# Performance work log

Measured on AMD Instinct MI355X. Metric: run time of the kernel, lower is better.

## Reference

```python
import jax, jax.numpy as jnp
import numpy as np

E = 2048        # embed_dim
H = 16          # num_heads
HKV = 4         # num_heads_kv (GQA)
D = 128         # head_dim
DCONV = 4       # causal depthwise conv width
ROT_DIM = 128   # rotary_emb_dim (= head_dim, full rotation)
ROT_BASE = 10000.0
QKV_DIM = D * (H + 2 * HKV)  # 3072
B, S = 2, 2048


def setup_inputs() -> dict:
    key = jax.random.key(0)
    ks = jax.random.split(key, 7)
    return {
        "x": jax.random.normal(ks[0], (B, S, E), jnp.float32),
        "W_in": jax.random.normal(ks[1], (E, QKV_DIM), jnp.float32) * 0.02,
        "b_in": jax.random.normal(ks[2], (QKV_DIM,), jnp.float32) * 0.02,
        "conv_w": jax.random.normal(ks[3], (QKV_DIM, DCONV), jnp.float32) * 0.1,
        "conv_b": jax.random.normal(ks[4], (QKV_DIM,), jnp.float32) * 0.02,
        "W_out": jax.random.normal(ks[5], (E, E), jnp.float32) * 0.02,
        "b_out": jax.random.normal(ks[6], (E,), jnp.float32) * 0.02,
    }


def _rotary_cos_sin(seqlen, dtype):
    # flash_attn RotaryEmbedding: inv_freq over even indices
    inv_freq = 1.0 / (ROT_BASE ** (np.arange(0, ROT_DIM, 2, dtype=np.float32) / ROT_DIM))
    t = np.arange(seqlen, dtype=np.float32)
    freqs = np.outer(t, inv_freq)                      # [S, ROT_DIM/2]
    return jnp.asarray(np.cos(freqs), dtype), jnp.asarray(np.sin(freqs), dtype)


def _apply_rotary(xh, cos, sin):
    # non-interleaved: rotate halves of the first ROT_DIM dims. xh: [B,S,h,D]
    x1 = xh[..., : ROT_DIM // 2]
    x2 = xh[..., ROT_DIM // 2 : ROT_DIM]
    c = cos[None, :, None, :]
    s = sin[None, :, None, :]
    rot = jnp.concatenate([x1 * c - x2 * s, x2 * c + x1 * s], axis=-1)
    return jnp.concatenate([rot, xh[..., ROT_DIM:]], axis=-1)


def _forward(x, W_in, b_in, conv_w, conv_b, W_out, b_out):
    b, s, _ = x.shape
    qkv = x @ W_in + b_in                              # [B,S,QKV_DIM]

    # causal depthwise conv1d (kernel DCONV, left-pad DCONV-1, trim right)
    xp = jnp.pad(qkv, ((0, 0), (DCONV - 1, 0), (0, 0)))
    conv = conv_b
    for k in range(DCONV):
        conv = conv + xp[:, k : k + s, :] * conv_w[:, k]
    qkv = conv                                         # [B,S,QKV_DIM]

    q, kv = jnp.split(qkv, [H * D], axis=-1)
    q = q.reshape(b, s, H, D)
    kv = kv.reshape(b, s, 2, HKV, D)
    k, v = kv[:, :, 0], kv[:, :, 1]                    # [B,S,HKV,D]

    cos, sin = _rotary_cos_sin(s, x.dtype)
    q = _apply_rotary(q, cos, sin)
    k = _apply_rotary(k, cos, sin)

    # GQA: repeat kv heads
    rep = H // HKV
    k = jnp.repeat(k, rep, axis=2)                     # [B,S,H,D]
    v = jnp.repeat(v, rep, axis=2)

    scale = 1.0 / np.sqrt(D)
    scores = jnp.einsum("bqhd,bkhd->bhqk", q, k) * scale
    causal = jnp.tril(jnp.ones((s, s), bool))
    scores = jnp.where(causal[None, None], scores, jnp.finfo(scores.dtype).min)
    probs = jax.nn.softmax(scores, axis=-1)
    ctx = jnp.einsum("bhqk,bkhd->bqhd", probs, v)      # [B,S,H,D]

    return ctx.reshape(b, s, H * D) @ W_out + b_out    # [B,S,E]


def reference(x, W_in, b_in, conv_w, conv_b, W_out, b_out):
    return _forward(x, W_in, b_in, conv_w, conv_b, W_out, b_out)
```

## Files before the change

### kernel.cpp

```cpp
#include <hip/hip_runtime.h>
#include <hip/hip_bf16.h>

#define B_    2
#define S_    2048
#define E_    2048
#define H_    16
#define HKV_  4
#define D_    128
#define QKV_  3072

#define LOG2E  1.4426950408889634f
#define SCALE  0.08838834764831845f
#define SL     0.127517431f

typedef __attribute__((ext_vector_type(8))) short short8;
typedef __attribute__((ext_vector_type(4))) float floatx4;

typedef __attribute__((address_space(1))) const unsigned int gu32;
typedef __attribute__((address_space(3))) unsigned int lu32;

__device__ __forceinline__ void load_lds16(const unsigned short* g, unsigned short* l) {
    __builtin_amdgcn_global_load_lds((gu32*)g, (lu32*)l, 16, 0, 0);
}

__device__ __forceinline__ float b2f(unsigned short u) {
    union { unsigned int i; float f; } v; v.i = ((unsigned int)u) << 16; return v.f;
}
__device__ __forceinline__ unsigned short f2b(float f) {
    union { float f; unsigned int i; } v; v.f = f;
    unsigned int r = v.i + 0x7FFFu + ((v.i >> 16) & 1u);
    return (unsigned short)(r >> 16);
}
__device__ __forceinline__ unsigned int fbits(float f) {
    union { float f; unsigned int i; } v; v.f = f; return v.i;
}
__device__ __forceinline__ float bits2f(unsigned int i) {
    union { unsigned int i; float f; } v; v.i = i; return v.f;
}

__global__ __launch_bounds__(256) void cvt_f32_bf16(
    const float* __restrict__ src, unsigned short* __restrict__ dst, int n)
{
    int i = (blockIdx.x * 256 + threadIdx.x) * 4;
    if (i + 3 < n) {
        float4 v = *(const float4*)&src[i];
        ushort4 o;
        o.x = f2b(v.x); o.y = f2b(v.y); o.z = f2b(v.z); o.w = f2b(v.w);
        *(ushort4*)&dst[i] = o;
    }
}

__global__ __launch_bounds__(256) void transpose_f32_bf16(
    const float* __restrict__ src, unsigned short* __restrict__ dst,
    int R, int C)
{
    __shared__ unsigned short tile[32][33];
    const int c0 = blockIdx.x * 32, r0 = blockIdx.y * 32;
    const int tx = threadIdx.x, ty = threadIdx.y;
    #pragma unroll
    for (int i = 0; i < 4; i++)
        tile[ty + 8 * i][tx] = f2b(src[(size_t)(r0 + ty + 8 * i) * C + c0 + tx]);
    __syncthreads();
    #pragma unroll
    for (int i = 0; i < 4; i++)
        dst[(size_t)(c0 + ty + 8 * i) * R + r0 + tx] = tile[tx][ty + 8 * i];
}

__global__ __launch_bounds__(256) void transpose_bf16(
    const unsigned short* __restrict__ src, unsigned short* __restrict__ dst,
    int R, int C)
{
    __shared__ unsigned short tile[32][33];
    const size_t boff = (size_t)blockIdx.z * R * C;
    src += boff; dst += boff;
    const int c0 = blockIdx.x * 32, r0 = blockIdx.y * 32;
    const int tx = threadIdx.x, ty = threadIdx.y;
    #pragma unroll
    for (int i = 0; i < 4; i++)
        tile[ty + 8 * i][tx] = src[(size_t)(r0 + ty + 8 * i) * C + c0 + tx];
    __syncthreads();
    #pragma unroll
    for (int i = 0; i < 4; i++)
        dst[(size_t)(c0 + ty + 8 * i) * R + r0 + tx] = tile[tx][ty + 8 * i];
}

template<int OUTF32>
__global__ __launch_bounds__(256) void gemm_bt(
    const unsigned short* __restrict__ A, const unsigned short* __restrict__ Bt,
    const float* __restrict__ bias, void* __restrict__ Cv,
    int M, int N, int K)
{
    __shared__ unsigned short As[128 * 64];
    __shared__ unsigned short Bs[128 * 64];
    const int tid = threadIdx.x;
    const int m0 = blockIdx.y * 128, n0 = blockIdx.x * 128;
    const int wave = tid >> 6, lane = tid & 63, ln = lane & 15, kq = lane >> 4;
    const int wm = (wave >> 1) * 64, wn = (wave & 1) * 64;

    floatx4 acc[4][4];
    #pragma unroll
    for (int i = 0; i < 4; i++)
        #pragma unroll
        for (int j = 0; j < 4; j++) {
            acc[i][j][0] = 0.f; acc[i][j][1] = 0.f; acc[i][j][2] = 0.f; acc[i][j][3] = 0.f;
        }

    const int lrow = lane >> 3;
    const int lcol = (lane & 7) * 8;

    for (int k0 = 0; k0 < K; k0 += 64) {
        __syncthreads();
        #pragma unroll
        for (int c = 0; c < 4; c++) {
            int rbase = wave * 32 + c * 8;
            int row = rbase + lrow;
            load_lds16(&A [(size_t)(m0 + row) * K + k0 + lcol], &As[rbase * 64]);
            load_lds16(&Bt[(size_t)(n0 + row) * K + k0 + lcol], &Bs[rbase * 64]);
        }
        __syncthreads();
        #pragma unroll
        for (int ks = 0; ks < 2; ks++) {
            short8 af[4], bg[4];
            #pragma unroll
            for (int i = 0; i < 4; i++)
                af[i] = *(const short8*)&As[(wm + i * 16 + ln) * 64 + ks * 32 + kq * 8];
            #pragma unroll
            for (int j = 0; j < 4; j++)
                bg[j] = *(const short8*)&Bs[(wn + j * 16 + ln) * 64 + ks * 32 + kq * 8];
            #pragma unroll
            for (int i = 0; i < 4; i++)
                #pragma unroll
                for (int j = 0; j < 4; j++)
                    acc[i][j] = __builtin_amdgcn_mfma_f32_16x16x32_bf16(af[i], bg[j], acc[i][j], 0, 0, 0);
        }
    }

    #pragma unroll
    for (int j = 0; j < 4; j++) {
        int col = n0 + wn + j * 16 + ln;
        float bv = bias[col];
        #pragma unroll
        for (int i = 0; i < 4; i++) {
            int rowb = m0 + wm + i * 16 + kq * 4;
            #pragma unroll
            for (int r = 0; r < 4; r++) {
                float val = acc[i][j][r] + bv;
                if (OUTF32) ((float*)Cv)[(size_t)(rowb + r) * N + col] = val;
                else ((unsigned short*)Cv)[(size_t)(rowb + r) * N + col] = f2b(val);
            }
        }
    }
}

__device__ __forceinline__ float conv_at(
    const unsigned short* __restrict__ qb, const float* __restrict__ cw,
    const float* __restrict__ cb, int s, int c)
{
    float acc = cb[c];
    const float* w = cw + c * 4;
    #pragma unroll
    for (int t = 0; t < 4; t++) {
        int sp = s - 3 + t;
        if (sp >= 0) acc += b2f(qb[(size_t)sp * QKV_ + c]) * w[t];
    }
    return acc;
}

__global__ __launch_bounds__(256) void conv_rot(
    const unsigned short* __restrict__ qkv, const float* __restrict__ cw,
    const float* __restrict__ cb, unsigned short* __restrict__ qo,
    unsigned short* __restrict__ ko, unsigned short* __restrict__ vo)
{
    const int bs = blockIdx.x;
    const int b = bs >> 11, s = bs & 2047;
    const unsigned short* qb = qkv + (size_t)b * S_ * QKV_;

    for (int it = threadIdx.x; it < 1792; it += 256) {
        if (it < 1280) {
            const int isq = it < 1024;
            const int rel = isq ? it : it - 1024;
            const int head = rel >> 6, d = rel & 63;
            const int c1 = (isq ? head * 128 : 2048 + head * 128) + d;
            float x1 = conv_at(qb, cw, cb, s, c1);
            float x2 = conv_at(qb, cw, cb, s, c1 + 64);
            float inv = exp2f((float)d * -0.2076205059304601f);
            float ang = (float)s * inv;
            float sn, cs;
            __sincosf(ang, &sn, &cs);
            float r1 = x1 * cs - x2 * sn;
            float r2 = x2 * cs + x1 * sn;
            unsigned short* dst = isq
                ? qo + ((size_t)(b * H_   + head) * S_ + s) * D_
                : ko + ((size_t)(b * HKV_ + head) * S_ + s) * D_;
            dst[d]      = f2b(r1);
            dst[d + 64] = f2b(r2);
        } else {
            const int idx = it - 1280;
            const int g = idx >> 7, d = idx & 127;
            float vv = conv_at(qb, cw, cb, s, 2560 + idx);
            vo[((size_t)(b * HKV_ + g) * S_ + s) * D_ + d] = f2b(vv);
        }
    }
}

__global__ __launch_bounds__(256, 4) void attn(
    const unsigned short* __restrict__ q, const unsigned short* __restrict__ k,
    const unsigned short* __restrict__ vT, unsigned short* __restrict__ ctx)
{
    __shared__ unsigned short Ks[64 * 128];
    __shared__ unsigned short Vs[128 * 64];
    __shared__ unsigned short Ps[4][16][64];

    const int h = blockIdx.x, qt = 31 - blockIdx.y, b = blockIdx.z, g = h >> 2;
    const int tid = threadIdx.x, wave = tid >> 6, lane = tid & 63;
    const int ln = lane & 15, kq = lane >> 4;

    const unsigned short* qh = q  + (size_t)(b * H_   + h) * S_ * D_;
    const unsigned short* kh = k  + (size_t)(b * HKV_ + g) * S_ * D_;
    const unsigned short* vh = vT + (size_t)(b * HKV_ + g) * D_ * S_;

    const int rK = (lane >> 4);
    const int pK = lane & 15;
    const int rV = (lane >> 3);
    const int pV = lane & 7;

    const int qrow0 = qt * 64 + wave * 16;

    short8 qf[4];
    #pragma unroll
    for (int f = 0; f < 4; f++)
        qf[f] = *(const short8*)&qh[(size_t)(qrow0 + ln) * D_ + f * 32 + kq * 8];

    floatx4 o[8];
    #pragma unroll
    for (int i = 0; i < 8; i++) { o[i][0] = 0.f; o[i][1] = 0.f; o[i][2] = 0.f; o[i][3] = 0.f; }
    float mr = -INFINITY, lr = 0.f;

    for (int kt = 0; kt <= qt; kt++) {
        __syncthreads();
        #pragma unroll
        for (int c = 0; c < 4; c++) {
            const int chunk = wave * 4 + c;
            int r  = chunk * 4 + rK;
            int gc = pK ^ (r & 15);
            load_lds16(&kh[(size_t)(kt * 64 + r) * D_ + gc * 8], &Ks[chunk * 512]);
            int rv = chunk * 8 + rV;
            int gv = pV ^ (rv & 7);
            load_lds16(&vh[(size_t)rv * S_ + kt * 64 + gv * 8], &Vs[chunk * 512]);
        }
        __syncthreads();

        floatx4 scv[4];
        #pragma unroll
        for (int nb = 0; nb < 4; nb++) { scv[nb][0]=0.f; scv[nb][1]=0.f; scv[nb][2]=0.f; scv[nb][3]=0.f; }
        #pragma unroll
        for (int ks = 0; ks < 4; ks++) {
            #pragma unroll
            for (int nb = 0; nb < 4; nb++) {
                short8 kf = *(const short8*)&Ks[(nb * 16 + ln) * 128 + (((ks * 4 + kq) ^ ln) * 8)];
                scv[nb] = __builtin_amdgcn_mfma_f32_16x16x32_bf16(kf, qf[ks], scv[nb], 0, 0, 0);
            }
        }

        if (kt == qt) {
            const int qloc = wave * 16 + ln;
            #pragma unroll
            for (int nb = 0; nb < 4; nb++)
                #pragma unroll
                for (int r = 0; r < 4; r++)
                    if (nb * 16 + kq * 4 + r > qloc) scv[nb][r] = -INFINITY;
        }

        float mx = -INFINITY;
        #pragma unroll
        for (int nb = 0; nb < 4; nb++) {
            float a0 = fmaxf(scv[nb][0], scv[nb][1]);
            float a1 = fmaxf(scv[nb][2], scv[nb][3]);
            mx = fmaxf(mx, fmaxf(a0, a1));
        }
        mx = fmaxf(mx, __shfl_xor(mx, 16));
        mx = fmaxf(mx, __shfl_xor(mx, 32));
        float mt = fmaxf(mr, mx);
        float al = exp2f((mr - mt) * SL);
        mr = mt;

        float rs = 0.f;
        #pragma unroll
        for (int nb = 0; nb < 4; nb++) {
            const int gct = 2 * nb + (kq >> 1);
            const int pbase = ((gct ^ (ln & 7)) << 3) + ((kq & 1) << 2);
            #pragma unroll
            for (int rr = 0; rr < 2; rr++) {
                unsigned int u0 = fbits(exp2f((scv[nb][2 * rr]     - mt) * SL));
                unsigned int u1 = fbits(exp2f((scv[nb][2 * rr + 1] - mt) * SL));
                rs += bits2f(u0 & 0xFFFF0000u) + bits2f(u1 & 0xFFFF0000u);
                *(unsigned int*)&Ps[wave][ln][pbase + 2 * rr] =
                    (u0 >> 16) | (u1 & 0xFFFF0000u);
            }
        }
        rs += __shfl_xor(rs, 16);
        rs += __shfl_xor(rs, 32);
        lr = lr * al + rs;

        float alr[4];
        #pragma unroll
        for (int r = 0; r < 4; r++) alr[r] = __shfl(al, kq * 4 + r);
        #pragma unroll
        for (int dn = 0; dn < 8; dn++)
            #pragma unroll
            for (int r = 0; r < 4; r++) o[dn][r] *= alr[r];

        short8 pa0 = *(const short8*)&Ps[wave][ln][(kq ^ (ln & 7)) << 3];
        short8 pa1 = *(const short8*)&Ps[wave][ln][((4 + kq) ^ (ln & 7)) << 3];
        #pragma unroll
        for (int dn = 0; dn < 8; dn++) {
            short8 b0 = *(const short8*)&Vs[(dn * 16 + ln) * 64 + ((kq ^ (ln & 7)) * 8)];
            o[dn] = __builtin_amdgcn_mfma_f32_16x16x32_bf16(pa0, b0, o[dn], 0, 0, 0);
            short8 b1 = *(const short8*)&Vs[(dn * 16 + ln) * 64 + (((4 + kq) ^ (ln & 7)) * 8)];
            o[dn] = __builtin_amdgcn_mfma_f32_16x16x32_bf16(pa1, b1, o[dn], 0, 0, 0);
        }
    }

    float lrr[4];
    #pragma unroll
    for (int r = 0; r < 4; r++) lrr[r] = 1.0f / __shfl(lr, kq * 4 + r);
    #pragma unroll
    for (int r = 0; r < 4; r++) {
        size_t rowoff = (size_t)(b * S_ + qt * 64 + wave * 16 + kq * 4 + r) * (H_ * D_) + h * D_;
        #pragma unroll
        for (int dn = 0; dn < 8; dn++)
            ctx[rowoff + dn * 16 + ln] = f2b(o[dn][r] * lrr[r]);
    }
}

extern "C" void kernel_launch(void* const* d_in, const int* in_sizes, int n_in,
                              void* d_out, int out_size, void* d_ws, size_t ws_size,
                              hipStream_t stream)
{
    const float* x     = (const float*)d_in[0];
    const float* W_in  = (const float*)d_in[1];
    const float* b_in  = (const float*)d_in[2];
    const float* cw    = (const float*)d_in[3];
    const float* cb    = (const float*)d_in[4];
    const float* W_out = (const float*)d_in[5];
    const float* b_out = (const float*)d_in[6];
    float* out = (float*)d_out;
    char* ws = (char*)d_ws;

    const size_t MB = 1024 * 1024;
    unsigned short* WtIn  = (unsigned short*)(ws);
    unsigned short* WtOut = (unsigned short*)(ws + 12 * MB);
    unsigned short* x16   = (unsigned short*)(ws + 20 * MB);
    unsigned short* qkv   = (unsigned short*)(ws + 36 * MB);
    unsigned short* qa    = (unsigned short*)(ws + 60 * MB);
    unsigned short* ka    = (unsigned short*)(ws + 76 * MB);
    unsigned short* va    = (unsigned short*)(ws + 80 * MB);
    unsigned short* vTa   = (unsigned short*)(ws + 84 * MB);
    unsigned short* ctx   = (unsigned short*)(ws + 20 * MB);

    dim3 tb(32, 8);
    hipLaunchKernelGGL(cvt_f32_bf16, dim3(8192), dim3(256), 0, stream, x, x16, 8388608);
    hipLaunchKernelGGL(transpose_f32_bf16, dim3(96, 64), tb, 0, stream, W_in,  WtIn,  2048, 3072);
    hipLaunchKernelGGL(transpose_f32_bf16, dim3(64, 64), tb, 0, stream, W_out, WtOut, 2048, 2048);
    hipLaunchKernelGGL(gemm_bt<0>, dim3(24, 32), dim3(256), 0, stream, x16, WtIn, b_in, (void*)qkv, 4096, 3072, 2048);
    hipLaunchKernelGGL(conv_rot, dim3(4096), dim3(256), 0, stream, qkv, cw, cb, qa, ka, va);
    hipLaunchKernelGGL(transpose_bf16, dim3(4, 64, 8), tb, 0, stream, va, vTa, 2048, 128);
    hipLaunchKernelGGL(attn, dim3(16, 32, 2), dim3(256), 0, stream, qa, ka, vTa, ctx);
    hipLaunchKernelGGL(gemm_bt<1>, dim3(16, 32), dim3(256), 0, stream, ctx, WtOut, b_out, (void*)out, 4096, 2048, 2048);
}
```

Baseline: 411.0 us.

## Replace GEMM with 8-wave double-buffered pipelined kernel with swizzled LDS

Replaces the simple 128x128 single-buffered GEMM with an 8-wave, 256-row tile kernel that double-buffers LDS. Global-to-LDS loads for the next K-tile are staged in four sub-units interleaved with MFMA work on quadrants of the current tile, using explicit vmcnt waits and barriers. It also XOR-swizzles LDS columns to avoid bank conflicts, remaps workgroup IDs for cache locality and raises MFMA priority. The aim is to hide memory latency and raise MFMA utilisation in both projection GEMMs. The cost is larger tiles, more LDS and register pressure, and fewer workgroups.

```diff
diff --git a/kernel.cpp b/kernel.cpp
--- a/kernel.cpp
+++ b/kernel.cpp
@@ -38,6 +38,19 @@
     union { unsigned int i; float f; } v; v.i = i; return v.f;
 }
 
+template<int N> __device__ __forceinline__ void waitcnt_vm() {
+    static_assert(N >= 0 && N <= 8, "vmcnt out of range");
+    if constexpr (N == 0) asm volatile("s_waitcnt vmcnt(0)" ::: "memory");
+    else if constexpr (N == 1) asm volatile("s_waitcnt vmcnt(1)" ::: "memory");
+    else if constexpr (N == 2) asm volatile("s_waitcnt vmcnt(2)" ::: "memory");
+    else if constexpr (N == 3) asm volatile("s_waitcnt vmcnt(3)" ::: "memory");
+    else if constexpr (N == 4) asm volatile("s_waitcnt vmcnt(4)" ::: "memory");
+    else if constexpr (N == 5) asm volatile("s_waitcnt vmcnt(5)" ::: "memory");
+    else if constexpr (N == 6) asm volatile("s_waitcnt vmcnt(6)" ::: "memory");
+    else if constexpr (N == 7) asm volatile("s_waitcnt vmcnt(7)" ::: "memory");
+    else asm volatile("s_waitcnt vmcnt(8)" ::: "memory");
+}
+
 __global__ __launch_bounds__(256) void cvt_f32_bf16(
     const float* __restrict__ src, unsigned short* __restrict__ dst, int n)
 {
@@ -84,67 +97,153 @@
         dst[(size_t)(c0 + ty + 8 * i) * R + r0 + tx] = tile[tx][ty + 8 * i];
 }
 
-template<int OUTF32>
-__global__ __launch_bounds__(256) void gemm_bt(
+template<int WR, int QR, int LX>
+__device__ __forceinline__ void stage_unit8(
+    const unsigned short* __restrict__ G, unsigned short* ls,
+    int uu, int g0, int K, int k0, int wave, int lane)
+{
+    #pragma unroll
+    for (int l = 0; l < LX; ++l) {
+        const int c    = wave * LX + l;
+        const int rr   = c / (QR / 8);
+        const int row0 = rr * WR + uu * QR + (c % (QR / 8)) * 8;
+        const int srow = row0 + (lane >> 3);
+        const int sg   = (lane & 7) ^ (lane >> 3);
+        load_lds16(&G[(size_t)(g0 + srow) * K + k0 + sg * 8], &ls[row0 * 64]);
+    }
+}
+
+template<int BN, int WM, int WN, int OUTF32>
+__global__ __launch_bounds__(512, 2) void gemm8(
     const unsigned short* __restrict__ A, const unsigned short* __restrict__ Bt,
     const float* __restrict__ bias, void* __restrict__ Cv,
     int M, int N, int K)
 {
-    __shared__ unsigned short As[128 * 64];
-    __shared__ unsigned short Bs[128 * 64];
-    const int tid = threadIdx.x;
-    const int m0 = blockIdx.y * 128, n0 = blockIdx.x * 128;
-    const int wave = tid >> 6, lane = tid & 63, ln = lane & 15, kq = lane >> 4;
-    const int wm = (wave >> 1) * 64, wn = (wave & 1) * 64;
-
-    floatx4 acc[4][4];
-    #pragma unroll
-    for (int i = 0; i < 4; i++)
-        #pragma unroll
-        for (int j = 0; j < 4; j++) {
-            acc[i][j][0] = 0.f; acc[i][j][1] = 0.f; acc[i][j][2] = 0.f; acc[i][j][3] = 0.f;
-        }
-
-    const int lrow = lane >> 3;
-    const int lcol = (lane & 7) * 8;
-
-    for (int k0 = 0; k0 < K; k0 += 64) {
-        __syncthreads();
-        #pragma unroll
-        for (int c = 0; c < 4; c++) {
-            int rbase = wave * 32 + c * 8;
-            int row = rbase + lrow;
-            load_lds16(&A [(size_t)(m0 + row) * K + k0 + lcol], &As[rbase * 64]);
-            load_lds16(&Bt[(size_t)(n0 + row) * K + k0 + lcol], &Bs[rbase * 64]);
-        }
-        __syncthreads();
-        #pragma unroll
-        for (int ks = 0; ks < 2; ks++) {
-            short8 af[4], bg[4];
-            #pragma unroll
-            for (int i = 0; i < 4; i++)
-                af[i] = *(const short8*)&As[(wm + i * 16 + ln) * 64 + ks * 32 + kq * 8];
-            #pragma unroll
-            for (int j = 0; j < 4; j++)
-                bg[j] = *(const short8*)&Bs[(wn + j * 16 + ln) * 64 + ks * 32 + kq * 8];
-            #pragma unroll
-            for (int i = 0; i < 4; i++)
-                #pragma unroll
-                for (int j = 0; j < 4; j++)
-                    acc[i][j] = __builtin_amdgcn_mfma_f32_16x16x32_bf16(af[i], bg[j], acc[i][j], 0, 0, 0);
-        }
-    }
-
-    #pragma unroll
-    for (int j = 0; j < 4; j++) {
-        int col = n0 + wn + j * 16 + ln;
-        float bv = bias[col];
-        #pragma unroll
-        for (int i = 0; i < 4; i++) {
-            int rowb = m0 + wm + i * 16 + kq * 4;
-            #pragma unroll
-            for (int r = 0; r < 4; r++) {
-                float val = acc[i][j][r] + bv;
+    constexpr int BM   = 256;
+    constexpr int WMR  = BM / WM, WNR = BN / WN;
+    constexpr int QMR  = WMR / 2, QNR = WNR / 2;
+    constexpr int FM   = QMR / 16, FN = QNR / 16;
+    constexpr int LA   = BM / 128, LB = BN / 128;
+    constexpr int TILE = (BM + BN) * 64;
+
+    __shared__ unsigned short lds[2 * TILE];
+
+    const int tid  = threadIdx.x;
+    const int wave = tid >> 6, lane = tid & 63;
+    const int ln   = lane & 15, kq = lane >> 4;
+    const int wm   = wave / WN, wn = wave % WN;
+
+    const int nwg = gridDim.x;
+    const int wg  = (blockIdx.x & 7) * (nwg >> 3) + (blockIdx.x >> 3);
+    const int nbn = N / BN;
+    const int m0  = (wg / nbn) * BM, n0 = (wg % nbn) * BN;
+
+    floatx4 acc[2 * FM][2 * FN];
+    #pragma unroll
+    for (int i = 0; i < 2 * FM; ++i)
+        #pragma unroll
+        for (int j = 0; j < 2 * FN; ++j) {
+            acc[i][j][0] = 0.f; acc[i][j][1] = 0.f;
+            acc[i][j][2] = 0.f; acc[i][j][3] = 0.f;
+        }
+
+    stage_unit8<WMR, QMR, LA>(A,  &lds[0],       0, m0, K, 0, wave, lane);
+    stage_unit8<WNR, QNR, LB>(Bt, &lds[BM * 64], 0, n0, K, 0, wave, lane);
+    stage_unit8<WNR, QNR, LB>(Bt, &lds[BM * 64], 1, n0, K, 0, wave, lane);
+    stage_unit8<WMR, QMR, LA>(A,  &lds[0],       1, m0, K, 0, wave, lane);
+    waitcnt_vm<LA + LB>();
+    __builtin_amdgcn_s_barrier();
+
+    const int NT = K >> 6;
+    int cur = 0;
+
+    for (int t = 0; t < NT - 1; ++t) {
+        const unsigned short* Asp = &lds[cur * TILE];
+        const unsigned short* Bsp = Asp + BM * 64;
+        unsigned short* Ssp = &lds[(cur ^ 1) * TILE];
+        const int k1 = (t + 1) << 6;
+        #pragma unroll
+        for (int p = 0; p < 4; ++p) {
+            const int qm = p >> 1, qn = p & 1;
+            short8 af[2][FM], bg[2][FN];
+            #pragma unroll
+            for (int ks = 0; ks < 2; ++ks) {
+                #pragma unroll
+                for (int i = 0; i < FM; ++i)
+                    af[ks][i] = *(const short8*)&Asp[(wm * WMR + qm * QMR + i * 16 + ln) * 64
+                                                     + (((ks * 4 + kq) ^ (ln & 7)) * 8)];
+                #pragma unroll
+                for (int j = 0; j < FN; ++j)
+                    bg[ks][j] = *(const short8*)&Bsp[(wn * WNR + qn * QNR + j * 16 + ln) * 64
+                                                     + (((ks * 4 + kq) ^ (ln & 7)) * 8)];
+            }
+            if (p == 0)      stage_unit8<WMR, QMR, LA>(A,  Ssp,           0, m0, K, k1, wave, lane);
+            else if (p == 1) stage_unit8<WNR, QNR, LB>(Bt, Ssp + BM * 64, 0, n0, K, k1, wave, lane);
+            else if (p == 2) stage_unit8<WNR, QNR, LB>(Bt, Ssp + BM * 64, 1, n0, K, k1, wave, lane);
+            else             stage_unit8<WMR, QMR, LA>(A,  Ssp,           1, m0, K, k1, wave, lane);
+            __builtin_amdgcn_s_barrier();
+            __builtin_amdgcn_s_setprio(1);
+            #pragma unroll
+            for (int ks = 0; ks < 2; ++ks)
+                #pragma unroll
+                for (int i = 0; i < FM; ++i)
+                    #pragma unroll
+                    for (int j = 0; j < FN; ++j)
+                        acc[qm * FM + i][qn * FN + j] = __builtin_amdgcn_mfma_f32_16x16x32_bf16(
+                            af[ks][i], bg[ks][j], acc[qm * FM + i][qn * FN + j], 0, 0, 0);
+            __builtin_amdgcn_s_setprio(0);
+            if (p == 0)      waitcnt_vm<2 * LA>();
+            else if (p == 1) waitcnt_vm<LA + LB>();
+            else if (p == 2) waitcnt_vm<LA + 2 * LB>();
+            else             waitcnt_vm<LA + LB>();
+            __builtin_amdgcn_s_barrier();
+        }
+        cur ^= 1;
+    }
+
+    asm volatile("s_waitcnt vmcnt(0)" ::: "memory");
+    __builtin_amdgcn_s_barrier();
+    {
+        const unsigned short* Asp = &lds[cur * TILE];
+        const unsigned short* Bsp = Asp + BM * 64;
+        #pragma unroll
+        for (int p = 0; p < 4; ++p) {
+            const int qm = p >> 1, qn = p & 1;
+            short8 af[2][FM], bg[2][FN];
+            #pragma unroll
+            for (int ks = 0; ks < 2; ++ks) {
+                #pragma unroll
+                for (int i = 0; i < FM; ++i)
+                    af[ks][i] = *(const short8*)&Asp[(wm * WMR + qm * QMR + i * 16 + ln) * 64
+                                                     + (((ks * 4 + kq) ^ (ln & 7)) * 8)];
+                #pragma unroll
+                for (int j = 0; j < FN; ++j)
+                    bg[ks][j] = *(const short8*)&Bsp[(wn * WNR + qn * QNR + j * 16 + ln) * 64
+                                                     + (((ks * 4 + kq) ^ (ln & 7)) * 8)];
+            }
+            __builtin_amdgcn_s_setprio(1);
+            #pragma unroll
+            for (int ks = 0; ks < 2; ++ks)
+                #pragma unroll
+                for (int i = 0; i < FM; ++i)
+                    #pragma unroll
+                    for (int j = 0; j < FN; ++j)
+                        acc[qm * FM + i][qn * FN + j] = __builtin_amdgcn_mfma_f32_16x16x32_bf16(
+                            af[ks][i], bg[ks][j], acc[qm * FM + i][qn * FN + j], 0, 0, 0);
+            __builtin_amdgcn_s_setprio(0);
+        }
+    }
+
+    #pragma unroll
+    for (int nj = 0; nj < 2 * FN; ++nj) {
+        const int col = n0 + wn * WNR + nj * 16 + ln;
+        const float bv = bias[col];
+        #pragma unroll
+        for (int mi = 0; mi < 2 * FM; ++mi) {
+            const int rowb = m0 + wm * WMR + mi * 16 + kq * 4;
+            #pragma unroll
+            for (int r = 0; r < 4; ++r) {
+                const float val = acc[mi][nj][r] + bv;
                 if (OUTF32) ((float*)Cv)[(size_t)(rowb + r) * N + col] = val;
                 else ((unsigned short*)Cv)[(size_t)(rowb + r) * N + col] = f2b(val);
             }
@@ -362,9 +461,11 @@
     hipLaunchKernelGGL(cvt_f32_bf16, dim3(8192), dim3(256), 0, stream, x, x16, 8388608);
     hipLaunchKernelGGL(transpose_f32_bf16, dim3(96, 64), tb, 0, stream, W_in,  WtIn,  2048, 3072);
     hipLaunchKernelGGL(transpose_f32_bf16, dim3(64, 64), tb, 0, stream, W_out, WtOut, 2048, 2048);
-    hipLaunchKernelGGL(gemm_bt<0>, dim3(24, 32), dim3(256), 0, stream, x16, WtIn, b_in, (void*)qkv, 4096, 3072, 2048);
+    hipLaunchKernelGGL((gemm8<256, 2, 4, 0>), dim3(192), dim3(512), 0, stream,
+                       x16, WtIn, b_in, (void*)qkv, 4096, 3072, 2048);
     hipLaunchKernelGGL(conv_rot, dim3(4096), dim3(256), 0, stream, qkv, cw, cb, qa, ka, va);
     hipLaunchKernelGGL(transpose_bf16, dim3(4, 64, 8), tb, 0, stream, va, vTa, 2048, 128);
     hipLaunchKernelGGL(attn, dim3(16, 32, 2), dim3(256), 0, stream, qa, ka, vTa, ctx);
-    hipLaunchKernelGGL(gemm_bt<1>, dim3(16, 32), dim3(256), 0, stream, ctx, WtOut, b_out, (void*)out, 4096, 2048, 2048);
-}
+    hipLaunchKernelGGL((gemm8<128, 4, 2, 1>), dim3(256), dim3(512), 0, stream,
+                       ctx, WtOut, b_out, (void*)out, 4096, 2048, 2048);
+}
```

After: 380.5 us. 1.08x faster.
